# Optimization experiments

Hardware: AMD Instinct MI355X
Metric: run time of the kernel (lower is better)

Reference implementation:

```python
import jax, jax.numpy as jnp
import numpy as np

# ---------- e3nn-style machinery, max_l = 1, real basis ----------
_EPS3 = np.zeros((3, 3, 3), dtype=np.float64)
_EPS3[0, 1, 2] = _EPS3[1, 2, 0] = _EPS3[2, 0, 1] = 1.0
_EPS3[0, 2, 1] = _EPS3[2, 1, 0] = _EPS3[1, 0, 2] = -1.0
W3J = {
    (0, 0, 0): np.ones((1, 1, 1)),
    (0, 1, 1): np.eye(3)[None, :, :] / np.sqrt(3.0),
    (1, 0, 1): np.eye(3)[:, None, :] / np.sqrt(3.0),
    (1, 1, 0): np.eye(3)[:, :, None] / np.sqrt(3.0),
    (1, 1, 1): _EPS3 / np.sqrt(6.0),
}

# irreps as (mul, l, parity)
IR_SH    = [(1, 0, 1), (1, 1, -1)]                      # 1x0e+1x1o (dim 4)
IR_INTER = [(4, 0, 1), (4, 0, -1), (2, 1, -1), (2, 1, 1)]  # gate.irreps_in (dim 20)
IR_GOUT  = [(2, 0, 1), (2, 0, -1), (2, 1, -1), (2, 1, 1)]  # gate.irreps_out (dim 16)
IR_OUT   = [(1, 1, -1), (1, 1, 1)]                      # 1x1o+1x1e (dim 6)

def _offsets(ir):
    off, o = [], 0
    for m, l, _ in ir:
        off.append(o)
        o += m * (2 * l + 1)
    return off, o

def build_tp(ir1, ir2, iro):
    """Fully-connected TP instructions: component irrep-norm, element path-norm."""
    fan = [0.0] * len(iro)
    paths = []
    for io, (mo, lo, po) in enumerate(iro):
        for i1, (m1, l1, p1) in enumerate(ir1):
            for i2, (m2, l2, p2) in enumerate(ir2):
                if p1 * p2 == po and abs(l1 - l2) <= lo <= l1 + l2:
                    paths.append((i1, i2, io))
                    fan[io] += m1 * m2
    ins, woff = [], 0
    for i1, i2, io in paths:
        m1, l1, _ = ir1[i1]; m2, l2, _ = ir2[i2]; mo, lo, _ = iro[io]
        alpha = float(np.sqrt((2 * lo + 1) / fan[io]))
        ins.append((i1, i2, io, alpha, woff))
        woff += m1 * m2 * mo
    return ins, woff

INS1, NUMEL1 = build_tp(IR_SH, IR_SH, IR_INTER)   # weight_numel = 14
INS2, NUMEL2 = build_tp(IR_GOUT, IR_SH, IR_OUT)   # weight_numel = 12

def tp_apply(ir1, ir2, iro, ins, x1, x2, w):
    off1, _ = _offsets(ir1); off2, _ = _offsets(ir2); offo, _ = _offsets(iro)
    lead = x1.shape[:-1]
    out = [None] * len(iro)
    for i1, i2, io, alpha, woff in ins:
        m1, l1, _ = ir1[i1]; m2, l2, _ = ir2[i2]; mo, lo, _ = iro[io]
        x1b = x1[..., off1[i1]:off1[i1] + m1 * (2 * l1 + 1)].reshape(lead + (m1, 2 * l1 + 1))
        x2b = x2[..., off2[i2]:off2[i2] + m2 * (2 * l2 + 1)].reshape(lead + (m2, 2 * l2 + 1))
        wb = w[..., woff:woff + m1 * m2 * mo].reshape(lead + (m1, m2, mo))
        C = jnp.asarray(W3J[(l1, l2, lo)], dtype=x1.dtype)
        blk = alpha * jnp.einsum('...ui,...vj,ijk,...uvw->...wk', x1b, x2b, C, wb)
        out[io] = blk if out[io] is None else out[io] + blk
    pieces = []
    for io, (mo, lo, _) in enumerate(iro):
        b = out[io] if out[io] is not None else jnp.zeros(lead + (mo, 2 * lo + 1), x1.dtype)
        pieces.append(b.reshape(lead + (mo * (2 * lo + 1),)))
    return jnp.concatenate(pieces, axis=-1)

def fc_net(x, w1, w2):
    # e3nn FullyConnectedNet: h = relu(x @ W1 / sqrt(fan_in)) * sqrt(2); out = h @ W2 / sqrt(fan)
    h = jax.nn.relu(x @ w1 / np.sqrt(w1.shape[0])) * np.sqrt(2.0)
    return h @ w2 / np.sqrt(w2.shape[0])

def gate_fn(x):
    # input irreps: [4x0e | 4x0o | 2x1o | 2x1e]; within 0e: 2 scalars + gates g1,g3; within 0o: 2 scalars + gates g2,g4
    lead = x.shape[:-1]
    se = jax.nn.relu(x[..., 0:2])
    ge = x[..., 2:4]
    so = jnp.abs(x[..., 4:6])
    go = x[..., 6:8]
    v1o = x[..., 8:14].reshape(lead + (2, 3))
    v1e = x[..., 14:20].reshape(lead + (2, 3))
    g1 = jax.nn.relu(ge[..., 0:1]); g3 = jax.nn.relu(ge[..., 1:2])
    g2 = jnp.tanh(go[..., 0:1]);    g4 = jnp.tanh(go[..., 1:2])
    v1o_out = jnp.concatenate([v1o[..., 0, :] * g1, v1o[..., 1, :] * g2], axis=-1)
    v1e_out = jnp.concatenate([v1e[..., 0, :] * g3, v1e[..., 1, :] * g4], axis=-1)
    return jnp.concatenate([se, so, v1o_out, v1e_out], axis=-1)  # [..., 16]

def sph_l1(d):
    # spherical harmonics l<=1, normalize=True, normalization='component' (e3nn l=1 order: y,z,x)
    n = jnp.sqrt(jnp.sum(d * d, axis=-1, keepdims=True) + 1e-12)
    u = d / n
    ones = jnp.ones(d.shape[:-1] + (1,), d.dtype)
    return jnp.concatenate([ones, np.sqrt(3.0) * u[..., [1, 2, 0]]], axis=-1)  # [..., 4]

def global_conv(ir1, iro, ins, nf, edge_attr, atten, normalizer, w1, w2):
    w = fc_net(atten, w1, w2)                                   # [B,N,N,numel]
    B, N = nf.shape[0], nf.shape[1]
    nfe = jnp.broadcast_to(nf[:, None, :, :], (B, N, N, nf.shape[-1]))  # node j at edge (i,j)
    ef = tp_apply(ir1, IR_SH, iro, ins, nfe, edge_attr, w)      # [B,N,N,dim_out]
    return jnp.sum(ef, axis=1) / normalizer

def _forward(attn_disp, attn_mask, coordinates, fc1_w1, fc1_w2, fc2_w1, fc2_w2):
    B, H, N, _ = attn_disp.shape
    normalizer = jnp.sqrt(jnp.sum((~jnp.isinf(attn_disp[:, 0])).astype(coordinates.dtype), axis=-1))[..., None]  # [B,N,1]
    ad = jnp.transpose(attn_disp, (0, 2, 3, 1))                 # [B,N,N,H]
    ad = jnp.where(jnp.isinf(ad), jnp.zeros((), ad.dtype), ad)
    # unit displacement (zero on diagonal)
    d = coordinates[:, :, None, :] - coordinates[:, None, :, :]
    d = d / (jnp.sqrt(jnp.sum(d * d, axis=-1, keepdims=True) + 1e-12) + 1e-5)
    edge_features = sph_l1(d)                                   # [B,N,N,4]
    nf = jnp.sum(edge_features, axis=1) / normalizer            # [B,N,4]
    nf = global_conv(IR_SH, IR_INTER, INS1, nf, edge_features, ad, normalizer, fc1_w1, fc1_w2)   # [B,N,20]
    nf = gate_fn(nf)                                            # [B,N,16]
    nf = global_conv(IR_GOUT, IR_OUT, INS2, nf, edge_features, ad, normalizer, fc2_w1, fc2_w2)   # [B,N,6]
    return ad, attn_mask, coordinates, nf, edge_features

def setup_inputs() -> dict:
    key = jax.random.key(0)
    ks = jax.random.split(key, 8)
    B, H, N = 4, 16, 512
    return {
        'attn_disp': jax.random.normal(ks[0], (B, H, N, N), jnp.float32),
        'attn_mask': jax.random.normal(ks[1], (B * H, N, N), jnp.float32),
        'coordinates': jax.random.normal(ks[2], (B, N, 3), jnp.float32),
        'fc1_w1': jax.random.normal(ks[3], (H, 2 * H), jnp.float32),
        'fc1_w2': jax.random.normal(ks[4], (2 * H, NUMEL1), jnp.float32),
        'fc2_w1': jax.random.normal(ks[5], (H, 2 * H), jnp.float32),
        'fc2_w2': jax.random.normal(ks[6], (2 * H, NUMEL2), jnp.float32),
    }

def reference(attn_disp, attn_mask, coordinates, fc1_w1, fc1_w2, fc2_w1, fc2_w2):
    return _forward(attn_disp, attn_mask, coordinates, fc1_w1, fc1_w2, fc2_w1, fc2_w2)
```

## Files before the change

kernel.cpp:

```cpp
#include <hip/hip_runtime.h>
#include <cmath>

#define NN 512

__device__ __forceinline__ int is_inf_f(float x) {
    return (__float_as_uint(x) & 0x7fffffffu) == 0x7f800000u;
}

template<int CTRL>
__device__ __forceinline__ float fdpp(float v) {
    return __int_as_float(__builtin_amdgcn_mov_dpp(__float_as_int(v), CTRL, 0xf, 0xf, false));
}
#define DPP_XOR1 0xB1
#define DPP_XOR2 0x4E

__device__ __forceinline__ void edge_vec(float ci0, float ci1, float ci2,
                                         float cj0, float cj1, float cj2,
                                         float& e0, float& e1, float& e2) {
    float d0 = ci0 - cj0, d1 = ci1 - cj1, d2 = ci2 - cj2;
    float den = sqrtf(d0*d0 + d1*d1 + d2*d2 + 1e-12f) + 1e-5f;
    float r = 1.0f / den;
    d0 *= r; d1 *= r; d2 *= r;
    float n = sqrtf(d0*d0 + d1*d1 + d2*d2 + 1e-12f);
    float s = 1.7320508075688772f / n;
    e0 = d1 * s;
    e1 = d2 * s;
    e2 = d0 * s;
}

__global__ __launch_bounds__(256) void k_trans(
    const float* __restrict__ disp, const float* __restrict__ coords,
    float* __restrict__ ad_out, float* __restrict__ adT_out,
    float* __restrict__ ef_out, float* __restrict__ ws_norm)
{
    __shared__ float L[256 * 20];
    const int blk = blockIdx.x;
    const int b   = blk >> 7;
    const int i0  = (blk & 127) << 2;
    const int tid = threadIdx.x;
    const int il  = tid >> 6;
    const int jl  = tid & 63;
    const int i   = i0 + il;
    const float ci0 = coords[(b*NN+i)*3+0];
    const float ci1 = coords[(b*NN+i)*3+1];
    const float ci2 = coords[(b*NN+i)*3+2];
    int cnt = 0;
    for (int ch = 0; ch < 8; ch++) {
        const int j = ch*64 + jl;
        float v[16];
        #pragma unroll
        for (int h = 0; h < 16; h++) {
            float x = disp[(size_t)((b*16+h)*NN + i)*NN + j];
            int bad = is_inf_f(x);
            if (h == 0) cnt += 1 - bad;
            v[h] = bad ? 0.0f : x;
        }
        float4* dst = (float4*)(ad_out + (size_t)((b*NN+i)*NN + j)*16);
        dst[0] = make_float4(v[0], v[1], v[2], v[3]);
        dst[1] = make_float4(v[4], v[5], v[6], v[7]);
        dst[2] = make_float4(v[8], v[9], v[10], v[11]);
        dst[3] = make_float4(v[12], v[13], v[14], v[15]);
        {
            const float cj0 = coords[(b*NN+j)*3+0];
            const float cj1 = coords[(b*NN+j)*3+1];
            const float cj2 = coords[(b*NN+j)*3+2];
            float e0, e1, e2;
            edge_vec(ci0, ci1, ci2, cj0, cj1, cj2, e0, e1, e2);
            ((float4*)ef_out)[(size_t)(b*NN+i)*NN + j] = make_float4(1.0f, e0, e1, e2);
        }
        {
            float4* Lr = (float4*)(L + tid*20);
            Lr[0] = make_float4(v[0], v[1], v[2], v[3]);
            Lr[1] = make_float4(v[4], v[5], v[6], v[7]);
            Lr[2] = make_float4(v[8], v[9], v[10], v[11]);
            Lr[3] = make_float4(v[12], v[13], v[14], v[15]);
        }
        __syncthreads();
        #pragma unroll
        for (int p = 0; p < 4; p++) {
            const int jj  = (tid >> 4) + p*16;
            const int f   = tid & 15;
            const int iw  = f >> 2, w4 = f & 3;
            const int row = iw*64 + jj;
            float4 val = *(const float4*)(L + row*20 + w4*4);
            ((float4*)adT_out)[(size_t)((b*NN + ch*64 + jj)*NN + (i0 + iw))*4 + w4] = val;
        }
        __syncthreads();
    }
    #pragma unroll
    for (int off = 32; off >= 1; off >>= 1) cnt += __shfl_xor(cnt, off);
    if (jl == 0) ws_norm[b*NN + i] = sqrtf((float)cnt);
}

__global__ __launch_bounds__(256) void k_reduce4(
    const float* __restrict__ adT, const float* __restrict__ coords,
    const float* __restrict__ wA, const float* __restrict__ wB,
    float* __restrict__ ws)
{
    __shared__ float4 E4[NN];
    __shared__ float4 R4[4*64];
    __shared__ float  sred[12];
    const int blk  = blockIdx.x;
    const int b    = blk >> 9, j = blk & 511;
    const int tid  = threadIdx.x;
    const int lane = tid & 63;
    const int wv   = tid >> 6;
    const float cj0 = coords[(b*NN+j)*3+0];
    const float cj1 = coords[(b*NN+j)*3+1];
    const float cj2 = coords[(b*NN+j)*3+2];
    float se0 = 0.f, se1 = 0.f, se2 = 0.f;
    #pragma unroll
    for (int r = 0; r < 2; r++) {
        const int i = r*256 + tid;
        const float ci0 = coords[(b*NN+i)*3+0];
        const float ci1 = coords[(b*NN+i)*3+1];
        const float ci2 = coords[(b*NN+i)*3+2];
        float e0, e1, e2;
        edge_vec(ci0, ci1, ci2, cj0, cj1, cj2, e0, e1, e2);
        E4[i] = make_float4(e0, e1, e2, 0.f);
        se0 += e0; se1 += e1; se2 += e2;
    }
    const float* __restrict__ Wsel = (lane < 32) ? wA : wB;
    const int q  = lane & 3;
    const int cb = lane & 28 & 31;
    float wq[4][4];
    #pragma unroll
    for (int x = 0; x < 4; x++)
        #pragma unroll
        for (int hh = 0; hh < 4; hh++)
            wq[x][hh] = Wsel[(4*q + hh)*32 + (cb | (x ^ q))];
    __syncthreads();
    const float* __restrict__ Arow = adT + (size_t)((b*NN + j) * NN) * 16;
    float acc0 = 0.f, acc1 = 0.f, acc2 = 0.f, acc3 = 0.f;
    const int ibase = wv * 128;
    #pragma unroll 8
    for (int k = 0; k < 128; k++) {
        const int i = ibase + k;
        const float4 a = ((const float4*)(Arow + (size_t)i * 16))[q];
        const float4 ev = E4[i];
        float P0, P1, P2, P3;
        P0 = a.x * wq[0][0];
        P0 = fmaf(a.y, wq[0][1], P0);
        P0 = fmaf(a.z, wq[0][2], P0);
        P0 = fmaf(a.w, wq[0][3], P0);
        P1 = a.x * wq[1][0];
        P1 = fmaf(a.y, wq[1][1], P1);
        P1 = fmaf(a.z, wq[1][2], P1);
        P1 = fmaf(a.w, wq[1][3], P1);
        P2 = a.x * wq[2][0];
        P2 = fmaf(a.y, wq[2][1], P2);
        P2 = fmaf(a.z, wq[2][2], P2);
        P2 = fmaf(a.w, wq[2][3], P2);
        P3 = a.x * wq[3][0];
        P3 = fmaf(a.y, wq[3][1], P3);
        P3 = fmaf(a.z, wq[3][2], P3);
        P3 = fmaf(a.w, wq[3][3], P3);
        const float n0 = P0 + fdpp<DPP_XOR1>(P1);
        const float n2 = P2 + fdpp<DPP_XOR1>(P3);
        const float t  = n0 + fdpp<DPP_XOR2>(n2);
        const float m = fmaxf(t, 0.f);
        acc0 += m;
        acc1 = fmaf(ev.x, m, acc1);
        acc2 = fmaf(ev.y, m, acc2);
        acc3 = fmaf(ev.z, m, acc3);
    }
    R4[wv*64 + lane] = make_float4(acc0, acc1, acc2, acc3);
    #pragma unroll
    for (int off = 1; off < 64; off <<= 1) {
        se0 += __shfl_xor(se0, off);
        se1 += __shfl_xor(se1, off);
        se2 += __shfl_xor(se2, off);
    }
    if (lane == 0) { sred[wv*3+0] = se0; sred[wv*3+1] = se1; sred[wv*3+2] = se2; }
    __syncthreads();
    {
        const int col = tid & 63, wq2 = tid >> 6;
        const float* Rf = (const float*)R4;
        float v = Rf[(0*64+col)*4 + wq2] + Rf[(1*64+col)*4 + wq2]
                + Rf[(2*64+col)*4 + wq2] + Rf[(3*64+col)*4 + wq2];
        v *= 0.35355339059327373f;
        float* accg = ws + 2048*4 + (size_t)blk*256;
        accg[((col >> 5)*4 + wq2)*32 + (col & 31)] = v;
    }
    if (tid == 0) {
        float* seg = ws + 2048 + blk*3;
        seg[0] = sred[0]+sred[3]+sred[6]+sred[9];
        seg[1] = sred[1]+sred[4]+sred[7]+sred[10];
        seg[2] = sred[2]+sred[5]+sred[8]+sred[11];
    }
}

__global__ __launch_bounds__(256) void k_final(
    const float* __restrict__ ws,
    const float* __restrict__ w2a,
    const float* __restrict__ w2b,
    float* __restrict__ nf_out,
    const float* __restrict__ mask, float* __restrict__ mask_out,
    const float* __restrict__ coords, float* __restrict__ coords_out)
{
    if (blockIdx.x >= 8) {
        const int cblk = blockIdx.x - 8;
        const float4* mi = (const float4*)mask;
        float4* mo = (float4*)mask_out;
        const size_t base = (size_t)cblk * 8192;
        #pragma unroll
        for (int r = 0; r < 32; r++) mo[base + r*256 + threadIdx.x] = mi[base + r*256 + threadIdx.x];
        if (cblk == 0) {
            for (int idx = threadIdx.x; idx < 4*NN*3; idx += 256) coords_out[idx] = coords[idx];
        }
        return;
    }
    const int bj = blockIdx.x*256 + threadIdx.x;
    const float inv = 1.0f / ws[bj];
    const float s  = 512.0f * inv;
    const float vv0 = ws[2048 + bj*3 + 0] * inv;
    const float vv1 = ws[2048 + bj*3 + 1] * inv;
    const float vv2 = ws[2048 + bj*3 + 2] * inv;
    const float* acc = ws + 2048*4 + (size_t)bj*256;
    const float ksc = 0.17677669529663687f;
    float S0[14], S1[3][14];
    #pragma unroll
    for (int cc = 0; cc < 14; cc++) { S0[cc]=0.f; S1[0][cc]=0.f; S1[1][cc]=0.f; S1[2][cc]=0.f; }
    for (int c = 0; c < 32; c++) {
        const float p = acc[c], q0 = acc[32+c], q1 = acc[64+c], q2 = acc[96+c];
        #pragma unroll
        for (int cc = 0; cc < 14; cc++) {
            const float w = w2a[c*14+cc];
            S0[cc]    = fmaf(p,  w, S0[cc]);
            S1[0][cc] = fmaf(q0, w, S1[0][cc]);
            S1[1][cc] = fmaf(q1, w, S1[1][cc]);
            S1[2][cc] = fmaf(q2, w, S1[2][cc]);
        }
    }
    #pragma unroll
    for (int cc = 0; cc < 14; cc++) { S0[cc]*=ksc; S1[0][cc]*=ksc; S1[1][cc]*=ksc; S1[2][cc]*=ksc; }
    const float is2 = 0.7071067811865476f;
    const float is3 = 0.5773502691896258f;
    float x0[4];
    #pragma unroll
    for (int k = 0; k < 4; k++)
        x0[k] = inv*is2*( s*S0[k] + is3*(vv0*S1[0][4+k] + vv1*S1[1][4+k] + vv2*S1[2][4+k]) );
    const float vv[3] = {vv0, vv1, vv2};
    float x8[3];
    #pragma unroll
    for (int k = 0; k < 3; k++)
        x8[k] = inv*is2*( s*S1[k][8] + vv[k]*S0[10] );
    const float E12_0=S1[0][12], E12_1=S1[1][12], E12_2=S1[2][12];
    float x14[3];
    x14[0] = inv*is2*(vv1*E12_2 - vv2*E12_1);
    x14[1] = inv*is2*(vv2*E12_0 - vv0*E12_2);
    x14[2] = inv*is2*(vv0*E12_1 - vv1*E12_0);
    const float a0 = fmaxf(x0[0],0.f), a1 = fmaxf(x0[1],0.f);
    const float g1 = fmaxf(x0[2],0.f), g3 = fmaxf(x0[3],0.f);
    const float p0=x8[0]*g1,  p1=x8[1]*g1,  p2=x8[2]*g1;
    const float q0_=x14[0]*g3, q1_=x14[1]*g3, q2_=x14[2]*g3;
    float T0[12], T1[3][12];
    #pragma unroll
    for (int cc = 0; cc < 12; cc++){ T0[cc]=0.f; T1[0][cc]=0.f; T1[1][cc]=0.f; T1[2][cc]=0.f; }
    const float* acc2 = acc + 128;
    for (int c = 0; c < 32; c++) {
        const float p = acc2[c], r0 = acc2[32+c], r1 = acc2[64+c], r2 = acc2[96+c];
        #pragma unroll
        for (int cc = 0; cc < 12; cc++) {
            const float w = w2b[c*12+cc];
            T0[cc]    = fmaf(p,  w, T0[cc]);
            T1[0][cc] = fmaf(r0, w, T1[0][cc]);
            T1[1][cc] = fmaf(r1, w, T1[1][cc]);
            T1[2][cc] = fmaf(r2, w, T1[2][cc]);
        }
    }
    #pragma unroll
    for (int cc = 0; cc < 12; cc++){ T0[cc]*=ksc; T1[0][cc]*=ksc; T1[1][cc]*=ksc; T1[2][cc]*=ksc; }
    const float is6  = 0.4082482904638631f;
    const float is12 = 0.28867513459481287f;
    const float E0[3] = {T1[0][0], T1[1][0], T1[2][0]};
    const float E1[3] = {T1[0][1], T1[1][1], T1[2][1]};
    const float E4[3] = {T1[0][4], T1[1][4], T1[2][4]};
    const float E8[3] = {T1[0][8], T1[1][8], T1[2][8]};
    const float cq0 = q1_*E4[2] - q2_*E4[1];
    const float cq1 = q2_*E4[0] - q0_*E4[2];
    const float cq2 = q0_*E4[1] - q1_*E4[0];
    const float cp0 = p1*E8[2] - p2*E8[1];
    const float cp1 = p2*E8[0] - p0*E8[2];
    const float cp2 = p0*E8[1] - p1*E8[0];
    float o[6];
    o[0] = inv*( is6*(a0*E0[0] + a1*E1[0]) + is6*p0*T0[2] + is12*cq0 );
    o[1] = inv*( is6*(a0*E0[1] + a1*E1[1]) + is6*p1*T0[2] + is12*cq1 );
    o[2] = inv*( is6*(a0*E0[2] + a1*E1[2]) + is6*p2*T0[2] + is12*cq2 );
    o[3] = inv*( is12*cp0 + is6*q0_*T0[10] );
    o[4] = inv*( is12*cp1 + is6*q1_*T0[10] );
    o[5] = inv*( is12*cp2 + is6*q2_*T0[10] );
    #pragma unroll
    for (int k = 0; k < 6; k++) nf_out[bj*6+k] = o[k];
}

extern "C" void kernel_launch(void* const* d_in, const int* in_sizes, int n_in,
                              void* d_out, int out_size, void* d_ws, size_t ws_size,
                              hipStream_t stream) {
    const float* disp   = (const float*)d_in[0];
    const float* mask   = (const float*)d_in[1];
    const float* coords = (const float*)d_in[2];
    const float* fc1w1  = (const float*)d_in[3];
    const float* fc1w2  = (const float*)d_in[4];
    const float* fc2w1  = (const float*)d_in[5];
    const float* fc2w2  = (const float*)d_in[6];
    float* out = (float*)d_out;
    float* ad_out     = out;
    float* mask_out   = out + 16777216;
    float* coords_out = out + 33554432;
    float* nf_out     = coords_out + 6144;
    float* ef_out     = nf_out + 12288;
    float* ws = (float*)d_ws;

    float* adT = mask_out;

    k_trans  <<<512,  256, 0, stream>>>(disp, coords, ad_out, adT, ef_out, ws);
    k_reduce4<<<2048, 256, 0, stream>>>(adT, coords, fc1w1, fc2w1, ws);
    k_final  <<<520,  256, 0, stream>>>(ws, fc1w2, fc2w2, nf_out,
                                        mask, mask_out, coords, coords_out);
}
```

Measured before the change: 358.6 us.

## Reuse each loaded adT float4 across all four output column groups per lane

In the per-node reduction, each lane group now handles four edge rows at a time and keeps weights for all 64 hidden columns (4 replicas x 16 weights) in registers. Each loaded float4 of the transposed attention tensor is used for four column groups instead of one, so there are four times fewer global loads for the same FMA work. Partial sums are combined across the four row groups with cross-lane shuffles at the end. This raises register pressure (64 weight registers plus 16 accumulators), which may cut occupancy.

```diff
diff --git a/kernel.cpp b/kernel.cpp
--- a/kernel.cpp
+++ b/kernel.cpp
@@ -92,7 +92,7 @@
     if (jl == 0) ws_norm[b*NN + i] = sqrtf((float)cnt);
 }
 
-__global__ __launch_bounds__(256) void k_reduce4(
+__global__ __launch_bounds__(256) void k_reduce5(
     const float* __restrict__ adT, const float* __restrict__ coords,
     const float* __restrict__ wA, const float* __restrict__ wB,
     float* __restrict__ ws)
@@ -105,6 +105,9 @@
     const int tid  = threadIdx.x;
     const int lane = tid & 63;
     const int wv   = tid >> 6;
+    const int q    = lane & 3;
+    const int qg   = (lane >> 2) & 3;
+    const int g    = lane >> 4;
     const float cj0 = coords[(b*NN+j)*3+0];
     const float cj1 = coords[(b*NN+j)*3+1];
     const float cj2 = coords[(b*NN+j)*3+2];
@@ -120,51 +123,75 @@
         E4[i] = make_float4(e0, e1, e2, 0.f);
         se0 += e0; se1 += e1; se2 += e2;
     }
-    const float* __restrict__ Wsel = (lane < 32) ? wA : wB;
-    const int q  = lane & 3;
-    const int cb = lane & 28 & 31;
-    float wq[4][4];
-    #pragma unroll
-    for (int x = 0; x < 4; x++)
-        #pragma unroll
-        for (int hh = 0; hh < 4; hh++)
-            wq[x][hh] = Wsel[(4*q + hh)*32 + (cb | (x ^ q))];
+    float wr[4][4][4];
+    #pragma unroll
+    for (int r = 0; r < 4; r++) {
+        const float* __restrict__ Wn = (r < 2) ? wA : wB;
+        const int base = 16*(r & 1) + 4*qg;
+        #pragma unroll
+        for (int x = 0; x < 4; x++) {
+            const int c = base + (x ^ q);
+            #pragma unroll
+            for (int hh = 0; hh < 4; hh++)
+                wr[r][x][hh] = Wn[(4*q + hh)*32 + c];
+        }
+    }
     __syncthreads();
     const float* __restrict__ Arow = adT + (size_t)((b*NN + j) * NN) * 16;
-    float acc0 = 0.f, acc1 = 0.f, acc2 = 0.f, acc3 = 0.f;
+    float acc[4][4];
+    #pragma unroll
+    for (int r = 0; r < 4; r++)
+        #pragma unroll
+        for (int w = 0; w < 4; w++) acc[r][w] = 0.f;
     const int ibase = wv * 128;
-    #pragma unroll 8
-    for (int k = 0; k < 128; k++) {
-        const int i = ibase + k;
-        const float4 a = ((const float4*)(Arow + (size_t)i * 16))[q];
+    #pragma unroll 4
+    for (int kk = 0; kk < 32; kk++) {
+        const int i = ibase + 4*kk + g;
+        const float4 a = *(const float4*)(Arow + (size_t)i * 16 + q*4);
         const float4 ev = E4[i];
-        float P0, P1, P2, P3;
-        P0 = a.x * wq[0][0];
-        P0 = fmaf(a.y, wq[0][1], P0);
-        P0 = fmaf(a.z, wq[0][2], P0);
-        P0 = fmaf(a.w, wq[0][3], P0);
-        P1 = a.x * wq[1][0];
-        P1 = fmaf(a.y, wq[1][1], P1);
-        P1 = fmaf(a.z, wq[1][2], P1);
-        P1 = fmaf(a.w, wq[1][3], P1);
-        P2 = a.x * wq[2][0];
-        P2 = fmaf(a.y, wq[2][1], P2);
-        P2 = fmaf(a.z, wq[2][2], P2);
-        P2 = fmaf(a.w, wq[2][3], P2);
-        P3 = a.x * wq[3][0];
-        P3 = fmaf(a.y, wq[3][1], P3);
-        P3 = fmaf(a.z, wq[3][2], P3);
-        P3 = fmaf(a.w, wq[3][3], P3);
-        const float n0 = P0 + fdpp<DPP_XOR1>(P1);
-        const float n2 = P2 + fdpp<DPP_XOR1>(P3);
-        const float t  = n0 + fdpp<DPP_XOR2>(n2);
-        const float m = fmaxf(t, 0.f);
-        acc0 += m;
-        acc1 = fmaf(ev.x, m, acc1);
-        acc2 = fmaf(ev.y, m, acc2);
-        acc3 = fmaf(ev.z, m, acc3);
-    }
-    R4[wv*64 + lane] = make_float4(acc0, acc1, acc2, acc3);
+        #pragma unroll
+        for (int r = 0; r < 4; r++) {
+            float P0, P1, P2, P3;
+            P0 = a.x * wr[r][0][0];
+            P0 = fmaf(a.y, wr[r][0][1], P0);
+            P0 = fmaf(a.z, wr[r][0][2], P0);
+            P0 = fmaf(a.w, wr[r][0][3], P0);
+            P1 = a.x * wr[r][1][0];
+            P1 = fmaf(a.y, wr[r][1][1], P1);
+            P1 = fmaf(a.z, wr[r][1][2], P1);
+            P1 = fmaf(a.w, wr[r][1][3], P1);
+            P2 = a.x * wr[r][2][0];
+            P2 = fmaf(a.y, wr[r][2][1], P2);
+            P2 = fmaf(a.z, wr[r][2][2], P2);
+            P2 = fmaf(a.w, wr[r][2][3], P2);
+            P3 = a.x * wr[r][3][0];
+            P3 = fmaf(a.y, wr[r][3][1], P3);
+            P3 = fmaf(a.z, wr[r][3][2], P3);
+            P3 = fmaf(a.w, wr[r][3][3], P3);
+            const float n0 = P0 + fdpp<DPP_XOR1>(P1);
+            const float n2 = P2 + fdpp<DPP_XOR1>(P3);
+            const float t  = n0 + fdpp<DPP_XOR2>(n2);
+            const float m  = fmaxf(t, 0.f);
+            acc[r][0] += m;
+            acc[r][1] = fmaf(ev.x, m, acc[r][1]);
+            acc[r][2] = fmaf(ev.y, m, acc[r][2]);
+            acc[r][3] = fmaf(ev.z, m, acc[r][3]);
+        }
+    }
+    #pragma unroll
+    for (int r = 0; r < 4; r++)
+        #pragma unroll
+        for (int w = 0; w < 4; w++) {
+            float v = acc[r][w];
+            v += __shfl_xor(v, 16);
+            v += __shfl_xor(v, 32);
+            acc[r][w] = v;
+        }
+    if (lane < 16) {
+        #pragma unroll
+        for (int r = 0; r < 4; r++)
+            R4[wv*64 + 16*r + lane] = make_float4(acc[r][0], acc[r][1], acc[r][2], acc[r][3]);
+    }
     #pragma unroll
     for (int off = 1; off < 64; off <<= 1) {
         se0 += __shfl_xor(se0, off);
@@ -315,7 +342,7 @@
     float* adT = mask_out;
 
     k_trans  <<<512,  256, 0, stream>>>(disp, coords, ad_out, adT, ef_out, ws);
-    k_reduce4<<<2048, 256, 0, stream>>>(adT, coords, fc1w1, fc2w1, ws);
+    k_reduce5<<<2048, 256, 0, stream>>>(adT, coords, fc1w1, fc2w1, ws);
     k_final  <<<520,  256, 0, stream>>>(ws, fc1w2, fc2w2, nf_out,
                                         mask, mask_out, coords, coords_out);
 }
```

Measured after the change: 373.6 us. 4.2% more time.

## Drop transposed adT scratch copy and read ad output column-wise in reduction

Applied to the files above, without the earlier changes.

The staging kernel no longer writes a transposed copy of the attention displacement through shared memory into the mask output buffer. The reduction kernel now reads the already-written ad output with a strided column access instead. The mask and coordinate copies move from the final kernel into the staging kernel, which now launches one block per row. This removes a 64 MB write and its LDS transpose with barriers, but the reduction's reads become strided by 32 KB per step, which may hurt locality.

```diff
diff --git a/kernel.cpp b/kernel.cpp
--- a/kernel.cpp
+++ b/kernel.cpp
@@ -28,25 +28,23 @@
     e2 = d0 * s;
 }
 
-__global__ __launch_bounds__(256) void k_trans(
-    const float* __restrict__ disp, const float* __restrict__ coords,
-    float* __restrict__ ad_out, float* __restrict__ adT_out,
-    float* __restrict__ ef_out, float* __restrict__ ws_norm)
+__global__ __launch_bounds__(256) void k_stage(
+    const float* __restrict__ disp, const float* __restrict__ mask,
+    const float* __restrict__ coords,
+    float* __restrict__ ad_out, float* __restrict__ mask_out,
+    float* __restrict__ coords_out, float* __restrict__ ef_out,
+    float* __restrict__ ws_norm)
 {
-    __shared__ float L[256 * 20];
     const int blk = blockIdx.x;
-    const int b   = blk >> 7;
-    const int i0  = (blk & 127) << 2;
+    const int b = blk >> 9, i = blk & 511;
     const int tid = threadIdx.x;
-    const int il  = tid >> 6;
-    const int jl  = tid & 63;
-    const int i   = i0 + il;
     const float ci0 = coords[(b*NN+i)*3+0];
     const float ci1 = coords[(b*NN+i)*3+1];
     const float ci2 = coords[(b*NN+i)*3+2];
     int cnt = 0;
-    for (int ch = 0; ch < 8; ch++) {
-        const int j = ch*64 + jl;
+    #pragma unroll
+    for (int r = 0; r < 2; r++) {
+        const int j = r*256 + tid;
         float v[16];
         #pragma unroll
         for (int h = 0; h < 16; h++) {
@@ -60,40 +58,33 @@
         dst[1] = make_float4(v[4], v[5], v[6], v[7]);
         dst[2] = make_float4(v[8], v[9], v[10], v[11]);
         dst[3] = make_float4(v[12], v[13], v[14], v[15]);
-        {
-            const float cj0 = coords[(b*NN+j)*3+0];
-            const float cj1 = coords[(b*NN+j)*3+1];
-            const float cj2 = coords[(b*NN+j)*3+2];
-            float e0, e1, e2;
-            edge_vec(ci0, ci1, ci2, cj0, cj1, cj2, e0, e1, e2);
-            ((float4*)ef_out)[(size_t)(b*NN+i)*NN + j] = make_float4(1.0f, e0, e1, e2);
-        }
-        {
-            float4* Lr = (float4*)(L + tid*20);
-            Lr[0] = make_float4(v[0], v[1], v[2], v[3]);
-            Lr[1] = make_float4(v[4], v[5], v[6], v[7]);
-            Lr[2] = make_float4(v[8], v[9], v[10], v[11]);
-            Lr[3] = make_float4(v[12], v[13], v[14], v[15]);
-        }
-        __syncthreads();
-        #pragma unroll
-        for (int p = 0; p < 4; p++) {
-            const int jj  = (tid >> 4) + p*16;
-            const int f   = tid & 15;
-            const int iw  = f >> 2, w4 = f & 3;
-            const int row = iw*64 + jj;
-            float4 val = *(const float4*)(L + row*20 + w4*4);
-            ((float4*)adT_out)[(size_t)((b*NN + ch*64 + jj)*NN + (i0 + iw))*4 + w4] = val;
-        }
-        __syncthreads();
-    }
-    #pragma unroll
-    for (int off = 32; off >= 1; off >>= 1) cnt += __shfl_xor(cnt, off);
-    if (jl == 0) ws_norm[b*NN + i] = sqrtf((float)cnt);
-}
-
-__global__ __launch_bounds__(256) void k_reduce4(
-    const float* __restrict__ adT, const float* __restrict__ coords,
+        const float cj0 = coords[(b*NN+j)*3+0];
+        const float cj1 = coords[(b*NN+j)*3+1];
+        const float cj2 = coords[(b*NN+j)*3+2];
+        float e0, e1, e2;
+        edge_vec(ci0, ci1, ci2, cj0, cj1, cj2, e0, e1, e2);
+        ((float4*)ef_out)[(size_t)(b*NN+i)*NN + j] = make_float4(1.0f, e0, e1, e2);
+    }
+    {
+        const float4* mi = (const float4*)mask;
+        float4* mo = (float4*)mask_out;
+        const size_t mbase = (size_t)blk * 2048;
+        #pragma unroll
+        for (int r = 0; r < 8; r++) mo[mbase + r*256 + tid] = mi[mbase + r*256 + tid];
+    }
+    if (blk == 0) {
+        for (int idx = tid; idx < 4*NN*3; idx += 256) coords_out[idx] = coords[idx];
+    }
+    #pragma unroll
+    for (int off = 32; off >= 1; off >>= 1) cnt += __shfl_down(cnt, off);
+    __shared__ int sredi[4];
+    if ((tid & 63) == 0) sredi[tid >> 6] = cnt;
+    __syncthreads();
+    if (tid == 0) ws_norm[blk] = sqrtf((float)(sredi[0]+sredi[1]+sredi[2]+sredi[3]));
+}
+
+__global__ __launch_bounds__(256) void k_reduceA(
+    const float* __restrict__ ad, const float* __restrict__ coords,
     const float* __restrict__ wA, const float* __restrict__ wB,
     float* __restrict__ ws)
 {
@@ -130,13 +121,13 @@
         for (int hh = 0; hh < 4; hh++)
             wq[x][hh] = Wsel[(4*q + hh)*32 + (cb | (x ^ q))];
     __syncthreads();
-    const float* __restrict__ Arow = adT + (size_t)((b*NN + j) * NN) * 16;
+    const float* __restrict__ Acol = ad + ((size_t)b*NN*NN + j) * 16;
     float acc0 = 0.f, acc1 = 0.f, acc2 = 0.f, acc3 = 0.f;
     const int ibase = wv * 128;
     #pragma unroll 8
     for (int k = 0; k < 128; k++) {
         const int i = ibase + k;
-        const float4 a = ((const float4*)(Arow + (size_t)i * 16))[q];
+        const float4 a = ((const float4*)(Acol + (size_t)i * (NN*16)))[q];
         const float4 ev = E4[i];
         float P0, P1, P2, P3;
         P0 = a.x * wq[0][0];
@@ -194,22 +185,8 @@
     const float* __restrict__ ws,
     const float* __restrict__ w2a,
     const float* __restrict__ w2b,
-    float* __restrict__ nf_out,
-    const float* __restrict__ mask, float* __restrict__ mask_out,
-    const float* __restrict__ coords, float* __restrict__ coords_out)
+    float* __restrict__ nf_out)
 {
-    if (blockIdx.x >= 8) {
-        const int cblk = blockIdx.x - 8;
-        const float4* mi = (const float4*)mask;
-        float4* mo = (float4*)mask_out;
-        const size_t base = (size_t)cblk * 8192;
-        #pragma unroll
-        for (int r = 0; r < 32; r++) mo[base + r*256 + threadIdx.x] = mi[base + r*256 + threadIdx.x];
-        if (cblk == 0) {
-            for (int idx = threadIdx.x; idx < 4*NN*3; idx += 256) coords_out[idx] = coords[idx];
-        }
-        return;
-    }
     const int bj = blockIdx.x*256 + threadIdx.x;
     const float inv = 1.0f / ws[bj];
     const float s  = 512.0f * inv;
@@ -312,10 +289,8 @@
     float* ef_out     = nf_out + 12288;
     float* ws = (float*)d_ws;
 
-    float* adT = mask_out;
-
-    k_trans  <<<512,  256, 0, stream>>>(disp, coords, ad_out, adT, ef_out, ws);
-    k_reduce4<<<2048, 256, 0, stream>>>(adT, coords, fc1w1, fc2w1, ws);
-    k_final  <<<520,  256, 0, stream>>>(ws, fc1w2, fc2w2, nf_out,
-                                        mask, mask_out, coords, coords_out);
-}
+    k_stage  <<<2048, 256, 0, stream>>>(disp, mask, coords, ad_out, mask_out,
+                                        coords_out, ef_out, ws);
+    k_reduceA<<<2048, 256, 0, stream>>>(ad_out, coords, fc1w1, fc2w1, ws);
+    k_final  <<<8,    256, 0, stream>>>(ws, fc1w2, fc2w2, nf_out);
+}
```

Result: faster. 332.9 us (-7.2%).
